# Kernel optimization log

Hardware: AMD Instinct MI355X
Metric: run time of the kernel (lower is better)

## Reference

```python
import jax, jax.numpy as jnp
import numpy as np

N, D, H, B, E = 100000, 256, 256, 128, 128
STEPS = 5


def setup_inputs() -> dict:
    key = jax.random.key(0)
    ks = jax.random.split(key, 16)
    w = lambda i, shape: (jax.random.normal(ks[i], shape, jnp.float32) * 0.05)
    inp = {
        "x": jax.random.normal(ks[0], (N, D), jnp.float32),
        "batch_idxs": jnp.sort(jax.random.randint(ks[1], (N,), 0, B)),
        # FNN: Linear(D,H) -> ELU -> Linear(H,H)
        "fnn_W1": w(2, (D, H)), "fnn_b1": jnp.zeros((H,), jnp.float32),
        "fnn_W2": w(3, (H, H)), "fnn_b2": jnp.zeros((H,), jnp.float32),
        # 3-layer LSTM, input 2H (layer 0) / H (layers 1,2), hidden H
        "Wih0": w(4, (4 * H, 2 * H)), "Whh0": w(5, (4 * H, H)),
        "bih0": jnp.zeros((4 * H,), jnp.float32), "bhh0": jnp.zeros((4 * H,), jnp.float32),
        "Wih1": w(6, (4 * H, H)), "Whh1": w(7, (4 * H, H)),
        "bih1": jnp.zeros((4 * H,), jnp.float32), "bhh1": jnp.zeros((4 * H,), jnp.float32),
        "Wih2": w(8, (4 * H, H)), "Whh2": w(9, (4 * H, H)),
        "bih2": jnp.zeros((4 * H,), jnp.float32), "bhh2": jnp.zeros((4 * H,), jnp.float32),
        # output Linear(2H, E)
        "out_W": w(10, (2 * H, E)), "out_b": jnp.zeros((E,), jnp.float32),
    }
    return inp


def _lstm_cell(xin, h, c, Wih, Whh, bih, bhh):
    gates = xin @ Wih.T + bih + h @ Whh.T + bhh  # (B, 4H)
    i, f, g, o = jnp.split(gates, 4, axis=-1)    # PyTorch gate order i,f,g,o
    c = jax.nn.sigmoid(f) * c + jax.nn.sigmoid(i) * jnp.tanh(g)
    h = jax.nn.sigmoid(o) * jnp.tanh(c)
    return h, c


def reference(x, batch_idxs, fnn_W1, fnn_b1, fnn_W2, fnn_b2,
              Wih0, Whh0, bih0, bhh0, Wih1, Whh1, bih1, bhh1,
              Wih2, Whh2, bih2, bhh2, out_W, out_b):
    # FNN (ELU between layers)
    hfeat = jax.nn.elu(x @ fnn_W1 + fnn_b1) @ fnn_W2 + fnn_b2  # (N, H)

    Wihs, Whhs = (Wih0, Wih1, Wih2), (Whh0, Whh1, Whh2)
    bihs, bhhs = (bih0, bih1, bih2), (bhh0, bhh1, bhh2)
    hs = [jnp.zeros((B, H), hfeat.dtype) for _ in range(3)]
    cs = [jnp.zeros((B, H), hfeat.dtype) for _ in range(3)]
    q_star = jnp.zeros((B, 2 * H), hfeat.dtype)

    for _ in range(STEPS):
        layer_in = q_star
        for l in range(3):
            hs[l], cs[l] = _lstm_cell(layer_in, hs[l], cs[l], Wihs[l], Whhs[l], bihs[l], bhhs[l])
            layer_in = hs[l]
        q = layer_in  # (B, H)
        # segment (per-graph) attention softmax over nodes
        e = jnp.sum(hfeat * q[batch_idxs], axis=-1)                     # (N,)
        m = jax.ops.segment_max(e, batch_idxs, num_segments=B)
        m = jnp.where(jnp.isfinite(m), m, 0.0)                          # guard empty segments
        ex = jnp.exp(e - m[batch_idxs])
        denom = jax.ops.segment_sum(ex, batch_idxs, num_segments=B) + 1e-16
        a = ex / denom[batch_idxs]                                      # (N,)
        r = jax.ops.segment_sum(a[:, None] * hfeat, batch_idxs, num_segments=B)  # (B, H)
        q_star = jnp.concatenate([q, r], axis=-1)                       # (B, 2H)

    return q_star @ out_W + out_b  # (B, E)
```

## Files before the change

### kernel.cpp

```cpp
#include <hip/hip_runtime.h>

#define NN 100000
#define NSTEP 5
#define LSTR 264

typedef unsigned short ushort_t;
typedef __attribute__((ext_vector_type(8))) short short8;
typedef __attribute__((ext_vector_type(4))) float floatx4;

__device__ __forceinline__ ushort_t f2bf(float f){
  union { float f; unsigned u; } v; v.f = f;
  unsigned r = v.u + 0x7fffu + ((v.u >> 16) & 1u);
  return (ushort_t)(r >> 16);
}
__device__ __forceinline__ float bf2f(ushort_t s){
  union { unsigned u; float f; } v; v.u = ((unsigned)s) << 16;
  return v.f;
}
__device__ __forceinline__ float sigf(float x){ return 1.0f/(1.0f+__expf(-x)); }

__global__ __launch_bounds__(512, 4) void fnn_fused(const float* __restrict__ x,
    const ushort_t* __restrict__ W1P, const float* __restrict__ b1,
    const ushort_t* __restrict__ W2P, const float* __restrict__ b2,
    ushort_t* __restrict__ hfeat, int M)
{
  __shared__ ushort_t buf[64 * LSTR];
  int tid = threadIdx.x;
  int w = tid >> 6, lane = tid & 63, qd = lane >> 4, r16 = lane & 15;
  int row0 = blockIdx.x * 64;
  int col0 = w * 32;

  {
    float4 xv[8];
    #pragma unroll
    for (int it = 0; it < 8; it++){
      int idx = it * 512 + tid;
      int rg = row0 + (idx >> 6); if (rg >= M) rg = M - 1;
      xv[it] = *(const float4*)(x + (size_t)rg * 256 + (idx & 63) * 4);
    }
    #pragma unroll
    for (int it = 0; it < 8; it++){
      int idx = it * 512 + tid;
      ushort4 pk = make_ushort4(f2bf(xv[it].x), f2bf(xv[it].y), f2bf(xv[it].z), f2bf(xv[it].w));
      *(ushort4*)&buf[(idx >> 6) * LSTR + (idx & 63) * 4] = pk;
    }
  }
  __syncthreads();

  floatx4 acc[4][2];

  #pragma unroll
  for (int i=0;i<4;i++)
    #pragma unroll
    for (int j=0;j<2;j++) acc[i][j] = (floatx4){0.f,0.f,0.f,0.f};

  #pragma unroll
  for (int kc = 0; kc < 8; kc++){
    short8 af[4], bfr[2];
    #pragma unroll
    for (int i=0;i<4;i++)
      af[i] = *(const short8*)&buf[(i*16 + r16) * LSTR + kc*32 + qd*8];
    #pragma unroll
    for (int j=0;j<2;j++)
      bfr[j] = *(const short8*)(W1P + (size_t)(((w*2 + j)*8 + kc)*64 + lane)*8);
    #pragma unroll
    for (int i=0;i<4;i++)
      #pragma unroll
      for (int j=0;j<2;j++)
        acc[i][j] = __builtin_amdgcn_mfma_f32_16x16x32_bf16(af[i], bfr[j], acc[i][j], 0, 0, 0);
  }
  __syncthreads();

  #pragma unroll
  for (int i=0;i<4;i++){
    #pragma unroll
    for (int j=0;j<2;j++){
      int col = col0 + j*16 + r16;
      float bb = b1[col];
      #pragma unroll
      for (int rr=0;rr<4;rr++){
        int row = i*16 + qd*4 + rr;
        float v = acc[i][j][rr] + bb;
        v = v > 0.f ? v : (__expf(v) - 1.0f);
        buf[row * LSTR + col] = f2bf(v);
      }
    }
  }
  __syncthreads();

  #pragma unroll
  for (int i=0;i<4;i++)
    #pragma unroll
    for (int j=0;j<2;j++) acc[i][j] = (floatx4){0.f,0.f,0.f,0.f};

  #pragma unroll
  for (int kc = 0; kc < 8; kc++){
    short8 af[4], bfr[2];
    #pragma unroll
    for (int i=0;i<4;i++)
      af[i] = *(const short8*)&buf[(i*16 + r16) * LSTR + kc*32 + qd*8];
    #pragma unroll
    for (int j=0;j<2;j++)
      bfr[j] = *(const short8*)(W2P + (size_t)(((w*2 + j)*8 + kc)*64 + lane)*8);
    #pragma unroll
    for (int i=0;i<4;i++)
      #pragma unroll
      for (int j=0;j<2;j++)
        acc[i][j] = __builtin_amdgcn_mfma_f32_16x16x32_bf16(af[i], bfr[j], acc[i][j], 0, 0, 0);
  }

  #pragma unroll
  for (int i=0;i<4;i++){
    #pragma unroll
    for (int j=0;j<2;j++){
      int col = col0 + j*16 + r16;
      float bb = b2[col];
      #pragma unroll
      for (int rr=0;rr<4;rr++){
        int row = row0 + i*16 + qd*4 + rr;
        if (row < M) hfeat[(size_t)row * 256 + col] = f2bf(acc[i][j][rr] + bb);
      }
    }
  }
}

__global__ __launch_bounds__(256) void lstm_layer(const ushort_t* __restrict__ A, int lda,
    const ushort_t* __restrict__ WcP, const float* __restrict__ bcp, int KC,
    float* __restrict__ c, ushort_t* __restrict__ dstA, int sA,
    ushort_t* __restrict__ dstB, int sB, float* __restrict__ qdst)
{
  __shared__ float sbuf[3][4][256];
  int tid = threadIdx.x, w = tid >> 6, lane = tid & 63, qd = lane >> 4, r16 = lane & 15;
  int m0 = (blockIdx.x & 7) * 16, nt = blockIdx.x >> 3;
  int kcq = KC >> 2;
  int kc0 = w * kcq;

  floatx4 acc[4];
  #pragma unroll
  for (int g=0; g<4; g++) acc[g] = (floatx4){0.f,0.f,0.f,0.f};

  const ushort_t* Ar = A + (size_t)(m0 + r16) * lda + qd * 8;
  for (int kc = kc0; kc < kc0 + kcq; kc++){
    short8 av = *(const short8*)(Ar + kc*32);
    #pragma unroll
    for (int g = 0; g < 4; g++){
      short8 bv = *(const short8*)(WcP + (size_t)((((g*16 + nt)*KC) + kc)*64 + lane)*8);
      acc[g] = __builtin_amdgcn_mfma_f32_16x16x32_bf16(av, bv, acc[g], 0, 0, 0);
    }
  }
  if (w){
    #pragma unroll
    for (int g=0; g<4; g++) *(floatx4*)&sbuf[w-1][g][lane*4] = acc[g];
  }
  __syncthreads();
  if (w == 0){
    #pragma unroll
    for (int g=0; g<4; g++)
      #pragma unroll
      for (int t=0; t<3; t++){
        floatx4 p = *(floatx4*)&sbuf[t][g][lane*4];
        acc[g] = acc[g] + p;
      }
    int h = nt*16 + r16;
    float bci = bcp[h], bcf = bcp[256+h], bcg = bcp[512+h], bco = bcp[768+h];
    #pragma unroll
    for (int rr=0; rr<4; rr++){
      int row = m0 + qd*4 + rr;
      float gi = acc[0][rr] + bci;
      float gf = acc[1][rr] + bcf;
      float gg = acc[2][rr] + bcg;
      float go = acc[3][rr] + bco;
      float cp = c[row*256 + h];
      float cn = sigf(gf)*cp + sigf(gi)*tanhf(gg);
      float hn = sigf(go)*tanhf(cn);
      c[row*256 + h] = cn;
      ushort_t hb = f2bf(hn);
      dstA[row*sA + h] = hb;
      dstB[row*sB + h] = hb;
      if (qdst) qdst[row*512 + h] = hn;
    }
  }
}

__global__ __launch_bounds__(256) void attn_onepass(const ushort_t* __restrict__ hfeat,
    const int* __restrict__ seg, const float* __restrict__ q_star,
    float* __restrict__ r_part, float* __restrict__ z_part)
{
  __shared__ float sred[4][260];
  int b = blockIdx.x >> 3, p = blockIdx.x & 7;
  int w = threadIdx.x >> 6, lane = threadIdx.x & 63;
  int s0 = seg[b], s1 = seg[b+1];
  int len = s1 - s0;
  int q0 = s0 + ((len * p) >> 3);
  int q1 = s0 + ((len * (p+1)) >> 3);

  float S0=0.f, S1=0.f, S2=0.f, S3=0.f, Z=0.f;

  int n = q0 + w;
  if (n < q1){
    float4 q = *(const float4*)(q_star + (size_t)b*512 + lane*4);
    #define LOADH(nn) (*(const ushort4*)(hfeat + (size_t)(nn)*256 + lane*4))
    ushort4 ha = LOADH(n);
    ushort4 hb = ha;
    if (n + 4 < q1) hb = LOADH(n + 4);
    for (; n < q1; n += 8){
      ushort4 hc = ha, hd = hb;
      if (n + 8  < q1) hc = LOADH(n + 8);
      if (n + 12 < q1) hd = LOADH(n + 12);
      float a0=bf2f(ha.x), a1=bf2f(ha.y), a2=bf2f(ha.z), a3=bf2f(ha.w);
      float da = a0*q.x + a1*q.y + a2*q.z + a3*q.w;
      float b0=0.f,b1=0.f,b2=0.f,b3=0.f, db=0.f;
      int vB = (n + 4) < q1;
      if (vB){
        b0=bf2f(hb.x); b1=bf2f(hb.y); b2=bf2f(hb.z); b3=bf2f(hb.w);
        db = b0*q.x + b1*q.y + b2*q.z + b3*q.w;
      }
      #pragma unroll
      for (int off = 32; off; off >>= 1){
        da += __shfl_xor(da, off);
        db += __shfl_xor(db, off);
      }
      float wa = __expf(da);
      Z += wa; S0 += wa*a0; S1 += wa*a1; S2 += wa*a2; S3 += wa*a3;
      if (vB){
        float wb = __expf(db);
        Z += wb; S0 += wb*b0; S1 += wb*b1; S2 += wb*b2; S3 += wb*b3;
      }
      ha = hc; hb = hd;
    }
    #undef LOADH
  }

  *(float4*)&sred[w][lane*4] = (float4){S0, S1, S2, S3};
  if (lane == 0) sred[w][256] = Z;
  __syncthreads();
  int f = threadIdx.x;
  if (f < 256){
    float v = sred[0][f] + sred[1][f] + sred[2][f] + sred[3][f];
    r_part[((size_t)p*128 + b)*256 + f] = v;
    if (f == 0)
      z_part[p*128 + b] = sred[0][256] + sred[1][256] + sred[2][256] + sred[3][256];
  }
}

__global__ __launch_bounds__(256) void attn_fin(const float* __restrict__ r_part,
    const float* __restrict__ z_part, float* __restrict__ q_star, ushort_t* __restrict__ xc0,
    const float* __restrict__ outW, const float* __restrict__ outb,
    float* __restrict__ out, int last)
{
  __shared__ float qs[512];
  int b = blockIdx.x, f = threadIdx.x;
  float s = 0.f, z = 0.f;
  #pragma unroll
  for (int t = 0; t < 8; t++){
    s += r_part[((size_t)(t*128 + b))*256 + f];
    z += z_part[t*128 + b];
  }
  float v = s / (z + 1e-16f);
  q_star[b*512 + 256 + f] = v;
  xc0[b*768 + 256 + f] = f2bf(v);
  if (last){
    qs[f] = q_star[b*512 + f];
    qs[256 + f] = v;
    __syncthreads();
    if (f < 128){
      float acc = outb[f];
      for (int k = 0; k < 512; k++) acc += qs[k] * outW[k*128 + f];
      out[b*128 + f] = acc;
    }
  }
}

__global__ void prep_all(const float* __restrict__ W1, const float* __restrict__ W2,
    const float* __restrict__ Wih0, const float* __restrict__ Whh0,
    const float* __restrict__ Wih1, const float* __restrict__ Whh1,
    const float* __restrict__ Wih2, const float* __restrict__ Whh2,
    const float* __restrict__ bih0, const float* __restrict__ bhh0,
    const float* __restrict__ bih1, const float* __restrict__ bhh1,
    const float* __restrict__ bih2, const float* __restrict__ bhh2,
    const int* __restrict__ bidx,
    ushort_t* __restrict__ W1P, ushort_t* __restrict__ W2P,
    ushort_t* __restrict__ Wc0P, ushort_t* __restrict__ Wc1P, ushort_t* __restrict__ Wc2P,
    float* __restrict__ c, ushort_t* __restrict__ xc, float* __restrict__ q_star,
    float* __restrict__ bc, int* __restrict__ seg)
{
  int i = blockIdx.x*256 + threadIdx.x;
  if (i < 131072){
    const float* W = (i < 65536) ? W1 : W2;
    ushort_t* P = (i < 65536) ? W1P : W2P;
    int r = i & 65535;
    int T = r >> 12, r2 = r & 4095;
    int kc = r2 >> 9, l = (r2 >> 3) & 63, j = r2 & 7;
    int k = kc*32 + ((l>>4)<<3) + j;
    int n = T*16 + (l & 15);
    P[r] = f2bf(W[k*256 + n]);
    return;
  }
  i -= 131072;
  if (i < 786432){
    int T = i / 12288, r2 = i - T*12288;
    int kc = r2 >> 9, l = (r2 >> 3) & 63, j = r2 & 7;
    int k = kc*32 + ((l>>4)<<3) + j;
    int g = T >> 4, n = (T & 15)*16 + (l & 15);
    int row = g*256 + n;
    Wc0P[i] = f2bf(k < 512 ? Wih0[row*512 + k] : Whh0[row*256 + (k - 512)]);
    return;
  }
  i -= 786432;
  if (i < 1048576){
    const float* Wih = (i < 524288) ? Wih1 : Wih2;
    const float* Whh = (i < 524288) ? Whh1 : Whh2;
    ushort_t* P = (i < 524288) ? Wc1P : Wc2P;
    int r = i & 524287;
    int T = r >> 13, r2 = r & 8191;
    int kc = r2 >> 9, l = (r2 >> 3) & 63, j = r2 & 7;
    int k = kc*32 + ((l>>4)<<3) + j;
    int g = T >> 4, n = (T & 15)*16 + (l & 15);
    int row = g*256 + n;
    P[r] = f2bf(k < 256 ? Wih[row*256 + k] : Whh[row*256 + (k - 256)]);
    return;
  }
  i -= 1048576;
  if (i < 98304) { c[i] = 0.f; return; }
  i -= 98304;
  if (i < 229376) { xc[i] = 0; return; }
  i -= 229376;
  if (i < 65536) { q_star[i] = 0.f; return; }
  i -= 65536;
  if (i < 3072) {
    int l = i >> 10, g = i & 1023;
    const float* bi = (l == 0) ? bih0 : ((l == 1) ? bih1 : bih2);
    const float* bh = (l == 0) ? bhh0 : ((l == 1) ? bhh1 : bhh2);
    bc[i] = bi[g] + bh[g];
    return;
  }
  i -= 3072;
  if (i < 129) {
    int lo = 0, hi = NN;
    while (lo < hi){ int mid = (lo + hi) >> 1; if (bidx[mid] < i) lo = mid + 1; else hi = mid; }
    seg[i] = lo;
    return;
  }
}

extern "C" void kernel_launch(void* const* d_in, const int* in_sizes, int n_in,
                              void* d_out, int out_size, void* d_ws, size_t ws_size,
                              hipStream_t stream)
{
  const float* x    = (const float*)d_in[0];
  const int*   bidx = (const int*)  d_in[1];
  const float* W1   = (const float*)d_in[2];
  const float* b1   = (const float*)d_in[3];
  const float* W2   = (const float*)d_in[4];
  const float* b2   = (const float*)d_in[5];
  const float* Wih0 = (const float*)d_in[6];
  const float* Whh0 = (const float*)d_in[7];
  const float* bih0 = (const float*)d_in[8];
  const float* bhh0 = (const float*)d_in[9];
  const float* Wih1 = (const float*)d_in[10];
  const float* Whh1 = (const float*)d_in[11];
  const float* bih1 = (const float*)d_in[12];
  const float* bhh1 = (const float*)d_in[13];
  const float* Wih2 = (const float*)d_in[14];
  const float* Whh2 = (const float*)d_in[15];
  const float* bih2 = (const float*)d_in[16];
  const float* bhh2 = (const float*)d_in[17];
  const float* outW = (const float*)d_in[18];
  const float* outb = (const float*)d_in[19];

  char* p = (char*)d_ws;
  auto alloc = [&](size_t bytes)->char*{ char* r = p; p += (bytes + 255) & ~(size_t)255; return r; };
  ushort_t* hfeat  = (ushort_t*)alloc((size_t)NN*256*2);
  ushort_t* W1P    = (ushort_t*)alloc(65536*2);
  ushort_t* W2P    = (ushort_t*)alloc(65536*2);
  ushort_t* Wc0P   = (ushort_t*)alloc(786432*2);
  ushort_t* Wc1P   = (ushort_t*)alloc(524288*2);
  ushort_t* Wc2P   = (ushort_t*)alloc(524288*2);
  float*    bc     = (float*)   alloc(3072*4);
  float*    c_all  = (float*)   alloc(98304*4);
  ushort_t* xc     = (ushort_t*)alloc(229376*2);
  float*    q_star = (float*)   alloc(65536*4);
  float*    r_part = (float*)   alloc(8*128*256*4);
  float*    z_part = (float*)   alloc(8*128*4);
  int*      seg    = (int*)     alloc(129*4);

  ushort_t* xc0 = xc;
  ushort_t* xc1 = xc + 98304;
  ushort_t* xc2 = xc + 163840;
  float* c0 = c_all, *c1 = c_all + 32768, *c2 = c_all + 65536;
  float* bc0 = bc, *bc1 = bc + 1024, *bc2 = bc + 2048;

  prep_all<<<9229, 256, 0, stream>>>(W1, W2, Wih0, Whh0, Wih1, Whh1, Wih2, Whh2,
                                     bih0, bhh0, bih1, bhh1, bih2, bhh2, bidx,
                                     W1P, W2P, Wc0P, Wc1P, Wc2P,
                                     c_all, xc, q_star, bc, seg);

  fnn_fused<<<1563, 512, 0, stream>>>(x, W1P, b1, W2P, b2, hfeat, NN);

  for (int s = 0; s < NSTEP; s++){
    lstm_layer<<<128, 256, 0, stream>>>(xc0, 768, Wc0P, bc0, 24, c0, xc0 + 512, 768, xc1, 512, nullptr);
    lstm_layer<<<128, 256, 0, stream>>>(xc1, 512, Wc1P, bc1, 16, c1, xc1 + 256, 512, xc2, 512, nullptr);
    lstm_layer<<<128, 256, 0, stream>>>(xc2, 512, Wc2P, bc2, 16, c2, xc2 + 256, 512, xc0, 768, q_star);
    attn_onepass<<<1024, 256, 0, stream>>>(hfeat, seg, q_star, r_part, z_part);
    attn_fin<<<128, 256, 0, stream>>>(r_part, z_part, q_star, xc0, outW, outb,
                                      (float*)d_out, s == NSTEP-1 ? 1 : 0);
  }
}
```

Measured before the change: 414.6 us.

## Make FNN kernel persistent with register-resident weights and double-buffered x tiles

The fused FNN kernel now processes 160 rows per block in five 32-row tiles. Both weight matrices' fragments and the biases are loaded into registers once per block rather than re-read from global memory for every tile. The next x tile is prefetched into registers while the current tile's MFMAs run, then written to a second shared buffer. Bounds checks are dropped, which relies on 100000 being an exact multiple of 160, and the higher register pressure lowers occupancy to 2 blocks per SIMD.

```diff
diff --git a/kernel.cpp b/kernel.cpp
--- a/kernel.cpp
+++ b/kernel.cpp
@@ -19,108 +19,134 @@
 }
 __device__ __forceinline__ float sigf(float x){ return 1.0f/(1.0f+__expf(-x)); }
 
-__global__ __launch_bounds__(512, 4) void fnn_fused(const float* __restrict__ x,
+__global__ __launch_bounds__(512, 2) void fnn_fused(const float* __restrict__ x,
     const ushort_t* __restrict__ W1P, const float* __restrict__ b1,
     const ushort_t* __restrict__ W2P, const float* __restrict__ b2,
-    ushort_t* __restrict__ hfeat, int M)
-{
-  __shared__ ushort_t buf[64 * LSTR];
+    ushort_t* __restrict__ hfeat)
+{
+  __shared__ ushort_t xbuf[2][32 * LSTR];
+  __shared__ ushort_t tbuf[32 * LSTR];
   int tid = threadIdx.x;
   int w = tid >> 6, lane = tid & 63, qd = lane >> 4, r16 = lane & 15;
-  int row0 = blockIdx.x * 64;
-  int col0 = w * 32;
-
-  {
-    float4 xv[8];
-    #pragma unroll
-    for (int it = 0; it < 8; it++){
-      int idx = it * 512 + tid;
-      int rg = row0 + (idx >> 6); if (rg >= M) rg = M - 1;
-      xv[it] = *(const float4*)(x + (size_t)rg * 256 + (idx & 63) * 4);
-    }
-    #pragma unroll
-    for (int it = 0; it < 8; it++){
-      int idx = it * 512 + tid;
-      ushort4 pk = make_ushort4(f2bf(xv[it].x), f2bf(xv[it].y), f2bf(xv[it].z), f2bf(xv[it].w));
-      *(ushort4*)&buf[(idx >> 6) * LSTR + (idx & 63) * 4] = pk;
-    }
+
+  short8 w1r[8][2], w2r[8][2];
+  #pragma unroll
+  for (int kc = 0; kc < 8; kc++)
+    #pragma unroll
+    for (int j = 0; j < 2; j++){
+      size_t off = (size_t)(((w*2 + j)*8 + kc)*64 + lane)*8;
+      w1r[kc][j] = *(const short8*)(W1P + off);
+      w2r[kc][j] = *(const short8*)(W2P + off);
+    }
+  float bb1[2], bb2[2];
+  #pragma unroll
+  for (int j = 0; j < 2; j++){
+    int col = w*32 + j*16 + r16;
+    bb1[j] = b1[col];
+    bb2[j] = b2[col];
+  }
+
+  size_t row0 = (size_t)blockIdx.x * 160;
+
+  float4 xv[4];
+  #pragma unroll
+  for (int it = 0; it < 4; it++){
+    int idx = it*512 + tid;
+    xv[it] = *(const float4*)(x + (row0 + (idx>>6))*256 + (idx&63)*4);
+  }
+  #pragma unroll
+  for (int it = 0; it < 4; it++){
+    int idx = it*512 + tid;
+    ushort4 pk = make_ushort4(f2bf(xv[it].x), f2bf(xv[it].y), f2bf(xv[it].z), f2bf(xv[it].w));
+    *(ushort4*)&xbuf[0][(idx>>6)*LSTR + (idx&63)*4] = pk;
   }
   __syncthreads();
 
-  floatx4 acc[4][2];
-
-  #pragma unroll
-  for (int i=0;i<4;i++)
-    #pragma unroll
-    for (int j=0;j<2;j++) acc[i][j] = (floatx4){0.f,0.f,0.f,0.f};
-
-  #pragma unroll
-  for (int kc = 0; kc < 8; kc++){
-    short8 af[4], bfr[2];
-    #pragma unroll
-    for (int i=0;i<4;i++)
-      af[i] = *(const short8*)&buf[(i*16 + r16) * LSTR + kc*32 + qd*8];
-    #pragma unroll
-    for (int j=0;j<2;j++)
-      bfr[j] = *(const short8*)(W1P + (size_t)(((w*2 + j)*8 + kc)*64 + lane)*8);
-    #pragma unroll
-    for (int i=0;i<4;i++)
-      #pragma unroll
-      for (int j=0;j<2;j++)
-        acc[i][j] = __builtin_amdgcn_mfma_f32_16x16x32_bf16(af[i], bfr[j], acc[i][j], 0, 0, 0);
-  }
-  __syncthreads();
-
-  #pragma unroll
-  for (int i=0;i<4;i++){
-    #pragma unroll
-    for (int j=0;j<2;j++){
-      int col = col0 + j*16 + r16;
-      float bb = b1[col];
-      #pragma unroll
-      for (int rr=0;rr<4;rr++){
-        int row = i*16 + qd*4 + rr;
-        float v = acc[i][j][rr] + bb;
-        v = v > 0.f ? v : (__expf(v) - 1.0f);
-        buf[row * LSTR + col] = f2bf(v);
-      }
-    }
-  }
-  __syncthreads();
-
-  #pragma unroll
-  for (int i=0;i<4;i++)
-    #pragma unroll
-    for (int j=0;j<2;j++) acc[i][j] = (floatx4){0.f,0.f,0.f,0.f};
-
-  #pragma unroll
-  for (int kc = 0; kc < 8; kc++){
-    short8 af[4], bfr[2];
-    #pragma unroll
-    for (int i=0;i<4;i++)
-      af[i] = *(const short8*)&buf[(i*16 + r16) * LSTR + kc*32 + qd*8];
-    #pragma unroll
-    for (int j=0;j<2;j++)
-      bfr[j] = *(const short8*)(W2P + (size_t)(((w*2 + j)*8 + kc)*64 + lane)*8);
-    #pragma unroll
-    for (int i=0;i<4;i++)
-      #pragma unroll
-      for (int j=0;j<2;j++)
-        acc[i][j] = __builtin_amdgcn_mfma_f32_16x16x32_bf16(af[i], bfr[j], acc[i][j], 0, 0, 0);
-  }
-
-  #pragma unroll
-  for (int i=0;i<4;i++){
-    #pragma unroll
-    for (int j=0;j<2;j++){
-      int col = col0 + j*16 + r16;
-      float bb = b2[col];
-      #pragma unroll
-      for (int rr=0;rr<4;rr++){
-        int row = row0 + i*16 + qd*4 + rr;
-        if (row < M) hfeat[(size_t)row * 256 + col] = f2bf(acc[i][j][rr] + bb);
-      }
-    }
+  int cur = 0;
+  for (int t = 0; t < 5; t++){
+    size_t rowt = row0 + t*32;
+    if (t < 4){
+      #pragma unroll
+      for (int it = 0; it < 4; it++){
+        int idx = it*512 + tid;
+        xv[it] = *(const float4*)(x + (rowt + 32 + (idx>>6))*256 + (idx&63)*4);
+      }
+    }
+
+    floatx4 acc[2][2];
+    #pragma unroll
+    for (int i=0;i<2;i++)
+      #pragma unroll
+      for (int j=0;j<2;j++) acc[i][j] = (floatx4){0.f,0.f,0.f,0.f};
+    #pragma unroll
+    for (int kc = 0; kc < 8; kc++){
+      short8 af[2];
+      #pragma unroll
+      for (int i=0;i<2;i++)
+        af[i] = *(const short8*)&xbuf[cur][(i*16 + r16)*LSTR + kc*32 + qd*8];
+      #pragma unroll
+      for (int i=0;i<2;i++)
+        #pragma unroll
+        for (int j=0;j<2;j++)
+          acc[i][j] = __builtin_amdgcn_mfma_f32_16x16x32_bf16(af[i], w1r[kc][j], acc[i][j], 0, 0, 0);
+    }
+
+    #pragma unroll
+    for (int i=0;i<2;i++){
+      #pragma unroll
+      for (int j=0;j<2;j++){
+        int col = w*32 + j*16 + r16;
+        #pragma unroll
+        for (int rr=0;rr<4;rr++){
+          int row = i*16 + qd*4 + rr;
+          float v = acc[i][j][rr] + bb1[j];
+          v = v > 0.f ? v : (__expf(v) - 1.0f);
+          tbuf[row * LSTR + col] = f2bf(v);
+        }
+      }
+    }
+    __syncthreads();
+
+    #pragma unroll
+    for (int i=0;i<2;i++)
+      #pragma unroll
+      for (int j=0;j<2;j++) acc[i][j] = (floatx4){0.f,0.f,0.f,0.f};
+    #pragma unroll
+    for (int kc = 0; kc < 8; kc++){
+      short8 af[2];
+      #pragma unroll
+      for (int i=0;i<2;i++)
+        af[i] = *(const short8*)&tbuf[(i*16 + r16)*LSTR + kc*32 + qd*8];
+      #pragma unroll
+      for (int i=0;i<2;i++)
+        #pragma unroll
+        for (int j=0;j<2;j++)
+          acc[i][j] = __builtin_amdgcn_mfma_f32_16x16x32_bf16(af[i], w2r[kc][j], acc[i][j], 0, 0, 0);
+    }
+
+    #pragma unroll
+    for (int i=0;i<2;i++){
+      #pragma unroll
+      for (int j=0;j<2;j++){
+        int col = w*32 + j*16 + r16;
+        #pragma unroll
+        for (int rr=0;rr<4;rr++){
+          size_t row = rowt + i*16 + qd*4 + rr;
+          hfeat[row * 256 + col] = f2bf(acc[i][j][rr] + bb2[j]);
+        }
+      }
+    }
+
+    if (t < 4){
+      #pragma unroll
+      for (int it = 0; it < 4; it++){
+        int idx = it*512 + tid;
+        ushort4 pk = make_ushort4(f2bf(xv[it].x), f2bf(xv[it].y), f2bf(xv[it].z), f2bf(xv[it].w));
+        *(ushort4*)&xbuf[cur^1][(idx>>6)*LSTR + (idx&63)*4] = pk;
+      }
+    }
+    __syncthreads();
+    cur ^= 1;
   }
 }
 
@@ -189,8 +215,7 @@
   __shared__ float sred[4][260];
   int b = blockIdx.x >> 3, p = blockIdx.x & 7;
   int w = threadIdx.x >> 6, lane = threadIdx.x & 63;
-  int s0 = seg[b], s1 = seg[b+1];
-  int len = s1 - s0;
+  int s0 = seg[b], s1 = seg[b+1], len = s1 - s0;
   int q0 = s0 + ((len * p) >> 3);
   int q1 = s0 + ((len * (p+1)) >> 3);
 
@@ -395,7 +420,7 @@
                                      W1P, W2P, Wc0P, Wc1P, Wc2P,
                                      c_all, xc, q_star, bc, seg);
 
-  fnn_fused<<<1563, 512, 0, stream>>>(x, W1P, b1, W2P, b2, hfeat, NN);
+  fnn_fused<<<625, 512, 0, stream>>>(x, W1P, b1, W2P, b2, hfeat);
 
   for (int s = 0; s < NSTEP; s++){
     lstm_layer<<<128, 256, 0, stream>>>(xc0, 768, Wc0P, bc0, 24, c0, xc0 + 512, 768, xc1, 512, nullptr);
```

After: 408.9 us. No clear change (-1.4%).
